# Kernel tuning notes

Hardware: AMD Instinct MI355X
Metric: run time of the kernel (lower is better)

## Reference

```python
import jax, jax.numpy as jnp
import numpy as np

N_NODES = 50000


def _gin_conv(x, src, dst, w1, b1, w2, b2):
    # sum-aggregate neighbor features: agg[i] = sum_{(j->i) in E} x[j]
    agg = jax.ops.segment_sum(x[src], dst, num_segments=N_NODES)
    h = x + agg  # eps = 0 (PyG GINConv default, not trainable)
    h = jnp.maximum(h @ w1 + b1, 0.0) @ w2 + b2
    return h


def setup_inputs() -> dict:
    key = jax.random.key(0)
    ks = jax.random.split(key, 10)
    d_in, d_h, d_out = 128, 256, 2
    E = 600000
    x = jax.random.normal(ks[0], (N_NODES, d_in), dtype=jnp.float32)
    edge_index = jax.random.randint(ks[1], (2, E), 0, N_NODES, dtype=jnp.int64)
    s = lambda k, sh: jax.random.normal(k, sh, dtype=jnp.float32) * (1.0 / np.sqrt(sh[0]))
    return {
        "x": x,
        "edge_index": edge_index,
        "w1": s(ks[2], (d_in, d_h)), "b1": jnp.zeros((d_h,), jnp.float32),
        "w2": s(ks[3], (d_h, d_h)), "b2": jnp.zeros((d_h,), jnp.float32),
        "w3": s(ks[4], (d_h, d_h)), "b3": jnp.zeros((d_h,), jnp.float32),
        "w4": s(ks[5], (d_h, d_out)), "b4": jnp.zeros((d_out,), jnp.float32),
    }


def reference(x, edge_index, w1, b1, w2, b2, w3, b3, w4, b4):
    src, dst = edge_index[0], edge_index[1]
    h = _gin_conv(x, src, dst, w1, b1, w2, b2)
    h = jnp.maximum(h, 0.0)  # F.relu between the two GINConv layers
    h = _gin_conv(h, src, dst, w3, b3, w4, b4)
    return jax.nn.log_softmax(h, axis=1)
```

## Files before the change

### kernel.cpp

```cpp
#include <hip/hip_runtime.h>
#include <hip/hip_bf16.h>


typedef __attribute__((ext_vector_type(8))) short bf16x8;
typedef __attribute__((ext_vector_type(4))) float f32x4;

static __device__ __forceinline__ unsigned short f2bf(float f) {
    unsigned int u = __float_as_uint(f);
    unsigned int r = (u + 0x7fffu + ((u >> 16) & 1u)) >> 16;
    return (unsigned short)r;
}
static __device__ __forceinline__ float bf2f(unsigned short s) {
    return __uint_as_float(((unsigned int)s) << 16);
}
static __device__ __forceinline__ float bflo(unsigned int u) {
    return __uint_as_float(u << 16);
}
static __device__ __forceinline__ float bfhi(unsigned int u) {
    return __uint_as_float(u & 0xffff0000u);
}

#define S1 136
#define S2 264

__global__ __launch_bounds__(256) void degree_kernel(
    const int* __restrict__ dst, int* __restrict__ deg, int E)
{
    const int e = blockIdx.x * 256 + threadIdx.x;
    if (e < E) atomicAdd(&deg[dst[e]], 1);
}

__global__ __launch_bounds__(256) void block_sum_kernel(
    const int* __restrict__ deg, int* __restrict__ bsum, int M)
{
    const int b = blockIdx.x, t = threadIdx.x;
    const int idx = b * 1024 + t * 4;
    int s = 0;
    if (idx + 3 < M) {
        const int4 v = *(const int4*)(deg + idx);
        s = v.x + v.y + v.z + v.w;
    } else {
        #pragma unroll
        for (int i = 0; i < 4; ++i) if (idx + i < M) s += deg[idx + i];
    }
    #pragma unroll
    for (int off = 32; off > 0; off >>= 1) s += __shfl_down(s, off);
    __shared__ int ws[4];
    if ((t & 63) == 0) ws[t >> 6] = s;
    __syncthreads();
    if (t == 0) bsum[b] = ws[0] + ws[1] + ws[2] + ws[3];
}

__global__ __launch_bounds__(64) void scan_partials_kernel(
    const int* __restrict__ bsum, int* __restrict__ boff, int nB)
{
    const int t = threadIdx.x;
    const int v = (t < nB) ? bsum[t] : 0;
    int inc = v;
    #pragma unroll
    for (int off = 1; off < 64; off <<= 1) {
        const int u = __shfl_up(inc, off);
        if (t >= off) inc += u;
    }
    if (t < nB) boff[t] = inc - v;
}

__global__ __launch_bounds__(256) void scan_blocks_kernel(
    const int* __restrict__ deg, const int* __restrict__ boff,
    int* __restrict__ rowptr, int* __restrict__ cur, int M, int E)
{
    const int b = blockIdx.x, t = threadIdx.x;
    const int idx = b * 1024 + t * 4;
    int4 d = make_int4(0, 0, 0, 0);
    if (idx + 3 < M) {
        d = *(const int4*)(deg + idx);
    } else {
        if (idx + 0 < M) d.x = deg[idx + 0];
        if (idx + 1 < M) d.y = deg[idx + 1];
        if (idx + 2 < M) d.z = deg[idx + 2];
        if (idx + 3 < M) d.w = deg[idx + 3];
    }
    const int tot = d.x + d.y + d.z + d.w;
    const int lane = t & 63, wid = t >> 6;
    int inc = tot;
    #pragma unroll
    for (int off = 1; off < 64; off <<= 1) {
        const int u = __shfl_up(inc, off);
        if (lane >= off) inc += u;
    }
    __shared__ int wsum[4];
    if (lane == 63) wsum[wid] = inc;
    __syncthreads();
    int woff = 0;
    #pragma unroll
    for (int w = 0; w < 4; ++w) if (w < wid) woff += wsum[w];
    int p = boff[b] + woff + (inc - tot);
    if (idx + 0 < M) { rowptr[idx + 0] = p; cur[idx + 0] = p; } p += d.x;
    if (idx + 1 < M) { rowptr[idx + 1] = p; cur[idx + 1] = p; } p += d.y;
    if (idx + 2 < M) { rowptr[idx + 2] = p; cur[idx + 2] = p; } p += d.z;
    if (idx + 3 < M) { rowptr[idx + 3] = p; cur[idx + 3] = p; }
    if (b == 0 && t == 0) rowptr[M] = E;
}

__global__ __launch_bounds__(256) void fill_kernel(
    const int* __restrict__ src, const int* __restrict__ dst,
    int* __restrict__ cur, int* __restrict__ srcs, int E)
{
    const int e = blockIdx.x * 256 + threadIdx.x;
    if (e >= E) return;
    const int p = atomicAdd(&cur[dst[e]], 1);
    srcs[p] = src[e];
}

__global__ __launch_bounds__(256) void cvt_bf16_kernel(
    const float* __restrict__ in, short* __restrict__ outb, int n4)
{
    const int i = (blockIdx.x * 256 + threadIdx.x);
    if (i >= n4) return;
    const float4 v = *(const float4*)(in + (size_t)i * 4);
    ushort4 o;
    o.x = f2bf(v.x); o.y = f2bf(v.y); o.z = f2bf(v.z); o.w = f2bf(v.w);
    *(ushort4*)(outb + (size_t)i * 4) = o;
}

__global__ __launch_bounds__(256) void transpose_cvt_kernel(
    const float* __restrict__ in, short* __restrict__ outb,
    int K, int N, int ostride)
{
    __shared__ float tile[32][33];
    const int k0 = blockIdx.x * 32;
    const int n0 = blockIdx.y * 32;
    const int tx = threadIdx.x & 31;
    const int ty = threadIdx.x >> 5;
    #pragma unroll
    for (int i = 0; i < 4; ++i)
        tile[ty + 8 * i][tx] = in[(size_t)(k0 + ty + 8 * i) * N + n0 + tx];
    __syncthreads();
    #pragma unroll
    for (int i = 0; i < 4; ++i)
        outb[(size_t)(n0 + ty + 8 * i) * ostride + k0 + tx] = (short)f2bf(tile[tx][ty + 8 * i]);
}

__global__ __launch_bounds__(256) void gather_add_d128(
    const short* __restrict__ feat,
    const int* __restrict__ rowptr, const int* __restrict__ srcs,
    short* __restrict__ outb, int M)
{
    const int row = blockIdx.x * 4 + (threadIdx.x >> 6);
    if (row >= M) return;
    const int o = (threadIdx.x & 63) * 2;
    const unsigned int u = *(const unsigned int*)(feat + (size_t)row * 128 + o);
    float a0 = bflo(u), a1 = bfhi(u);
    const int jb = rowptr[row], je = rowptr[row + 1];
    int j = jb;
    for (; j + 4 <= je; j += 4) {
        const int s0 = srcs[j + 0];
        const int s1 = srcs[j + 1];
        const int s2 = srcs[j + 2];
        const int s3 = srcs[j + 3];
        const unsigned int v0 = *(const unsigned int*)(feat + (size_t)s0 * 128 + o);
        const unsigned int v1 = *(const unsigned int*)(feat + (size_t)s1 * 128 + o);
        const unsigned int v2 = *(const unsigned int*)(feat + (size_t)s2 * 128 + o);
        const unsigned int v3 = *(const unsigned int*)(feat + (size_t)s3 * 128 + o);
        a0 += bflo(v0); a1 += bfhi(v0);
        a0 += bflo(v1); a1 += bfhi(v1);
        a0 += bflo(v2); a1 += bfhi(v2);
        a0 += bflo(v3); a1 += bfhi(v3);
    }
    for (; j < je; ++j) {
        const int s = srcs[j];
        const unsigned int v = *(const unsigned int*)(feat + (size_t)s * 128 + o);
        a0 += bflo(v); a1 += bfhi(v);
    }
    const unsigned int up = (unsigned int)f2bf(a0) | ((unsigned int)f2bf(a1) << 16);
    *(unsigned int*)(outb + (size_t)row * S1 + o) = up;
}

__global__ __launch_bounds__(256) void gather_add_d256(
    const short* __restrict__ feat,
    const int* __restrict__ rowptr, const int* __restrict__ srcs,
    short* __restrict__ outb, int M)
{
    const int row = blockIdx.x * 4 + (threadIdx.x >> 6);
    if (row >= M) return;
    const int o = (threadIdx.x & 63) * 4;
    const uint2 u = *(const uint2*)(feat + (size_t)row * 256 + o);
    float a0 = bflo(u.x), a1 = bfhi(u.x);
    float a2 = bflo(u.y), a3 = bfhi(u.y);
    const int jb = rowptr[row], je = rowptr[row + 1];
    int j = jb;
    for (; j + 4 <= je; j += 4) {
        const int s0 = srcs[j + 0];
        const int s1 = srcs[j + 1];
        const int s2 = srcs[j + 2];
        const int s3 = srcs[j + 3];
        const uint2 v0 = *(const uint2*)(feat + (size_t)s0 * 256 + o);
        const uint2 v1 = *(const uint2*)(feat + (size_t)s1 * 256 + o);
        const uint2 v2 = *(const uint2*)(feat + (size_t)s2 * 256 + o);
        const uint2 v3 = *(const uint2*)(feat + (size_t)s3 * 256 + o);
        a0 += bflo(v0.x); a1 += bfhi(v0.x); a2 += bflo(v0.y); a3 += bfhi(v0.y);
        a0 += bflo(v1.x); a1 += bfhi(v1.x); a2 += bflo(v1.y); a3 += bfhi(v1.y);
        a0 += bflo(v2.x); a1 += bfhi(v2.x); a2 += bflo(v2.y); a3 += bfhi(v2.y);
        a0 += bflo(v3.x); a1 += bfhi(v3.x); a2 += bflo(v3.y); a3 += bfhi(v3.y);
    }
    for (; j < je; ++j) {
        const int s = srcs[j];
        const uint2 v = *(const uint2*)(feat + (size_t)s * 256 + o);
        a0 += bflo(v.x); a1 += bfhi(v.x); a2 += bflo(v.y); a3 += bfhi(v.y);
    }
    uint2 up;
    up.x = (unsigned int)f2bf(a0) | ((unsigned int)f2bf(a1) << 16);
    up.y = (unsigned int)f2bf(a2) | ((unsigned int)f2bf(a3) << 16);
    *(uint2*)(outb + (size_t)row * S2 + o) = up;
}

__global__ __launch_bounds__(256) void layer1_fused(
    const short* __restrict__ h1in,
    const short* __restrict__ w1t,
    const float* __restrict__ b1,
    const short* __restrict__ w2t,
    const float* __restrict__ b2,
    short* __restrict__ h1,
    int M)
{
    __shared__ short sT[64 * S2];
    const int tid  = threadIdx.x;
    const int lane = tid & 63;
    const int wid  = tid >> 6;
    const int r16  = lane & 15;
    const int q    = lane >> 4;
    const int tm   = blockIdx.x * 64;
    const int wn   = wid * 64;

    f32x4 acc[4][4];
    #pragma unroll
    for (int i = 0; i < 4; ++i)
        #pragma unroll
        for (int j = 0; j < 4; ++j)
            acc[i][j] = (f32x4)0.f;

    const short* Abase = h1in + (size_t)tm * S1;
    #pragma unroll
    for (int k0 = 0; k0 < 128; k0 += 32) {
        bf16x8 af[4], bfr[4];
        #pragma unroll
        for (int i = 0; i < 4; ++i)
            af[i] = *(const bf16x8*)(Abase + (size_t)(i * 16 + r16) * S1 + k0 + q * 8);
        #pragma unroll
        for (int j = 0; j < 4; ++j)
            bfr[j] = *(const bf16x8*)(w1t + (size_t)(wn + j * 16 + r16) * S1 + k0 + q * 8);
        #pragma unroll
        for (int i = 0; i < 4; ++i)
            #pragma unroll
            for (int j = 0; j < 4; ++j)
                acc[i][j] = __builtin_amdgcn_mfma_f32_16x16x32_bf16(af[i], bfr[j], acc[i][j], 0, 0, 0);
    }

    #pragma unroll
    for (int j = 0; j < 4; ++j) {
        const int col = wn + j * 16 + r16;
        const float bj = b1[col];
        #pragma unroll
        for (int i = 0; i < 4; ++i)
            #pragma unroll
            for (int r = 0; r < 4; ++r) {
                float v = fmaxf(acc[i][j][r] + bj, 0.f);
                sT[(i * 16 + q * 4 + r) * S2 + col] = (short)f2bf(v);
            }
    }
    __syncthreads();

    #pragma unroll
    for (int i = 0; i < 4; ++i)
        #pragma unroll
        for (int j = 0; j < 4; ++j)
            acc[i][j] = (f32x4)0.f;

    #pragma unroll
    for (int k0 = 0; k0 < 256; k0 += 32) {
        bf16x8 af[4], bfr[4];
        #pragma unroll
        for (int i = 0; i < 4; ++i)
            af[i] = *(const bf16x8*)(&sT[(i * 16 + r16) * S2 + k0 + q * 8]);
        #pragma unroll
        for (int j = 0; j < 4; ++j)
            bfr[j] = *(const bf16x8*)(w2t + (size_t)(wn + j * 16 + r16) * S2 + k0 + q * 8);
        #pragma unroll
        for (int i = 0; i < 4; ++i)
            #pragma unroll
            for (int j = 0; j < 4; ++j)
                acc[i][j] = __builtin_amdgcn_mfma_f32_16x16x32_bf16(af[i], bfr[j], acc[i][j], 0, 0, 0);
    }
    __syncthreads();

    #pragma unroll
    for (int j = 0; j < 4; ++j) {
        const int col = wn + j * 16 + r16;
        const float bj = b2[col];
        #pragma unroll
        for (int i = 0; i < 4; ++i)
            #pragma unroll
            for (int r = 0; r < 4; ++r) {
                float v = fmaxf(acc[i][j][r] + bj, 0.f);
                sT[(i * 16 + q * 4 + r) * S2 + col] = (short)f2bf(v);
            }
    }
    __syncthreads();

    #pragma unroll
    for (int c = 0; c < 8; ++c) {
        const int idx = tid + c * 256;
        const int row = idx >> 5;
        const int ch  = idx & 31;
        const int rg  = tm + row;
        if (rg < M) {
            const uint4 v = *(const uint4*)(&sT[row * S2 + ch * 8]);
            *(uint4*)(h1 + (size_t)rg * 256 + ch * 8) = v;
        }
    }
}

__global__ __launch_bounds__(256) void layer2_fused(
    const short* __restrict__ h2in,
    const short* __restrict__ w3t,
    const float* __restrict__ b3,
    const float* __restrict__ w4,
    const float* __restrict__ b4,
    float* __restrict__ out,
    int M)
{
    __shared__ short sT[64 * S2];
    const int tid  = threadIdx.x;
    const int lane = tid & 63;
    const int wid  = tid >> 6;
    const int r16  = lane & 15;
    const int q    = lane >> 4;
    const int tm   = blockIdx.x * 64;
    const int wn   = wid * 64;

    f32x4 acc[4][4];
    #pragma unroll
    for (int i = 0; i < 4; ++i)
        #pragma unroll
        for (int j = 0; j < 4; ++j)
            acc[i][j] = (f32x4)0.f;

    const short* Abase = h2in + (size_t)tm * S2;
    #pragma unroll
    for (int k0 = 0; k0 < 256; k0 += 32) {
        bf16x8 af[4], bfr[4];
        #pragma unroll
        for (int i = 0; i < 4; ++i)
            af[i] = *(const bf16x8*)(Abase + (size_t)(i * 16 + r16) * S2 + k0 + q * 8);
        #pragma unroll
        for (int j = 0; j < 4; ++j)
            bfr[j] = *(const bf16x8*)(w3t + (size_t)(wn + j * 16 + r16) * S2 + k0 + q * 8);
        #pragma unroll
        for (int i = 0; i < 4; ++i)
            #pragma unroll
            for (int j = 0; j < 4; ++j)
                acc[i][j] = __builtin_amdgcn_mfma_f32_16x16x32_bf16(af[i], bfr[j], acc[i][j], 0, 0, 0);
    }

    #pragma unroll
    for (int j = 0; j < 4; ++j) {
        const int col = wn + j * 16 + r16;
        const float bj = b3[col];
        #pragma unroll
        for (int i = 0; i < 4; ++i)
            #pragma unroll
            for (int r = 0; r < 4; ++r) {
                float v = fmaxf(acc[i][j][r] + bj, 0.f);
                sT[(i * 16 + q * 4 + r) * S2 + col] = (short)f2bf(v);
            }
    }
    __syncthreads();

    const int row = tid >> 2;
    const int qd  = tid & 3;
    const short* tp = &sT[row * S2 + qd * 64];
    const float* w4p = w4 + qd * 128;
    float s0 = 0.f, s1 = 0.f;
    #pragma unroll 8
    for (int k = 0; k < 64; ++k) {
        const float a = bf2f((unsigned short)tp[k]);
        const float2 w = *(const float2*)(w4p + 2 * k);
        s0 = fmaf(a, w.x, s0);
        s1 = fmaf(a, w.y, s1);
    }
    s0 += __shfl_down(s0, 2, 4);  s1 += __shfl_down(s1, 2, 4);
    s0 += __shfl_down(s0, 1, 4);  s1 += __shfl_down(s1, 1, 4);
    if (qd == 0) {
        const int rg = tm + row;
        if (rg < M) {
            s0 += b4[0];
            s1 += b4[1];
            const float m = fmaxf(s0, s1);
            const float l = logf(__expf(s0 - m) + __expf(s1 - m));
            float2 o;
            o.x = s0 - m - l;
            o.y = s1 - m - l;
            *(float2*)(out + (size_t)rg * 2) = o;
        }
    }
}

extern "C" void kernel_launch(void* const* d_in, const int* in_sizes, int n_in,
                              void* d_out, int out_size, void* d_ws, size_t ws_size,
                              hipStream_t stream)
{
    const float* x  = (const float*)d_in[0];
    const int*   ei = (const int*)d_in[1];
    const float* w1 = (const float*)d_in[2];
    const float* b1 = (const float*)d_in[3];
    const float* w2 = (const float*)d_in[4];
    const float* b2 = (const float*)d_in[5];
    const float* w3 = (const float*)d_in[6];
    const float* b3 = (const float*)d_in[7];
    const float* w4 = (const float*)d_in[8];
    const float* b4 = (const float*)d_in[9];

    const int DIN = 128, DH = 256;
    const int M = in_sizes[0] / DIN;
    const int E = in_sizes[1] / 2;
    const int* src = ei;
    const int* dst = ei + E;
    const int nB = (M + 1023) / 1024;

    int* deg    = (int*)d_ws;
    int* cur    = deg + M;
    int* rowptr = cur + M;
    int* bsum   = rowptr + (M + 1);
    int* boff   = bsum + 64;
    int* srcs   = boff + 64;
    size_t off = ((size_t)(3 * M + 1 + 128 + E) * sizeof(int) + 255) & ~(size_t)255;
    short* x_bf = (short*)((char*)d_ws + off);  off += (size_t)M * DIN * 2;
    off = (off + 255) & ~(size_t)255;
    short* h1in = (short*)((char*)d_ws + off);  off += (size_t)M * S1 * 2;
    off = (off + 255) & ~(size_t)255;
    short* h1   = (short*)((char*)d_ws + off);  off += (size_t)M * DH * 2;
    off = (off + 255) & ~(size_t)255;
    short* h2in = (short*)((char*)d_ws + off);  off += (size_t)M * S2 * 2;
    off = (off + 255) & ~(size_t)255;
    short* w1t  = (short*)((char*)d_ws + off);  off += (size_t)DH * S1 * 2;
    off = (off + 255) & ~(size_t)255;
    short* w2t  = (short*)((char*)d_ws + off);  off += (size_t)DH * S2 * 2;
    off = (off + 255) & ~(size_t)255;
    short* w3t  = (short*)((char*)d_ws + off);  off += (size_t)DH * S2 * 2;

    hipMemsetAsync(deg, 0, (size_t)M * sizeof(int), stream);
    degree_kernel<<<(E + 255) / 256, 256, 0, stream>>>(dst, deg, E);
    block_sum_kernel<<<nB, 256, 0, stream>>>(deg, bsum, M);
    scan_partials_kernel<<<1, 64, 0, stream>>>(bsum, boff, nB);
    scan_blocks_kernel<<<nB, 256, 0, stream>>>(deg, boff, rowptr, cur, M, E);
    fill_kernel<<<(E + 255) / 256, 256, 0, stream>>>(src, dst, cur, srcs, E);

    cvt_bf16_kernel<<<((M * DIN / 4) + 255) / 256, 256, 0, stream>>>(x, x_bf, M * DIN / 4);
    transpose_cvt_kernel<<<dim3(DIN / 32, DH / 32), 256, 0, stream>>>(w1, w1t, DIN, DH, S1);
    transpose_cvt_kernel<<<dim3(DH / 32, DH / 32), 256, 0, stream>>>(w2, w2t, DH, DH, S2);
    transpose_cvt_kernel<<<dim3(DH / 32, DH / 32), 256, 0, stream>>>(w3, w3t, DH, DH, S2);

    const int nblk = (M + 63) / 64;

    gather_add_d128<<<(M + 3) / 4, 256, 0, stream>>>(x_bf, rowptr, srcs, h1in, M);
    layer1_fused<<<nblk, 256, 0, stream>>>(h1in, w1t, b1, w2t, b2, h1, M);

    gather_add_d256<<<(M + 3) / 4, 256, 0, stream>>>(h1, rowptr, srcs, h2in, M);
    layer2_fused<<<nblk, 256, 0, stream>>>(h2in, w3t, b3, w4, b4, (float*)d_out, M);
}
```

Before: 296.4 us.

## Fuse neighbor gather-aggregation into layer MLP kernels via shared memory

Each fused layer kernel now gathers and sums neighbor features for its 64-row tile directly into shared memory, then runs the MFMA GEMMs from that buffer. This removes the separate gather kernels and the global round-trip of the aggregated h1in/h2in intermediates. The three weight transpose launches are merged into one 3D-grid launch, and launch bounds now request 4 blocks per CU. The tradeoff is that the irregular gather now runs inside the GEMM kernel with only 782 blocks, which may reduce the latency hiding the standalone gather kernels had from their larger grids.

```diff
diff --git a/kernel.cpp b/kernel.cpp
--- a/kernel.cpp
+++ b/kernel.cpp
@@ -123,13 +123,20 @@
     *(ushort4*)(outb + (size_t)i * 4) = o;
 }
 
-__global__ __launch_bounds__(256) void transpose_cvt_kernel(
-    const float* __restrict__ in, short* __restrict__ outb,
-    int K, int N, int ostride)
-{
+__global__ __launch_bounds__(256) void transpose_cvt3_kernel(
+    const float* __restrict__ w1, const float* __restrict__ w2, const float* __restrict__ w3,
+    short* __restrict__ w1t, short* __restrict__ w2t, short* __restrict__ w3t)
+{
+    const int z = blockIdx.z;
+    const float* in; short* outb; int K, ostride;
+    if (z == 0)      { in = w1; outb = w1t; K = 128; ostride = S1; }
+    else if (z == 1) { in = w2; outb = w2t; K = 256; ostride = S2; }
+    else             { in = w3; outb = w3t; K = 256; ostride = S2; }
+    const int N = 256;
+    const int k0 = blockIdx.x * 32;
+    if (k0 >= K) return;
+    const int n0 = blockIdx.y * 32;
     __shared__ float tile[32][33];
-    const int k0 = blockIdx.x * 32;
-    const int n0 = blockIdx.y * 32;
     const int tx = threadIdx.x & 31;
     const int ty = threadIdx.x >> 5;
     #pragma unroll
@@ -141,81 +148,9 @@
         outb[(size_t)(n0 + ty + 8 * i) * ostride + k0 + tx] = (short)f2bf(tile[tx][ty + 8 * i]);
 }
 
-__global__ __launch_bounds__(256) void gather_add_d128(
-    const short* __restrict__ feat,
+__global__ __launch_bounds__(256, 4) void layer1_fused(
+    const short* __restrict__ x_bf,
     const int* __restrict__ rowptr, const int* __restrict__ srcs,
-    short* __restrict__ outb, int M)
-{
-    const int row = blockIdx.x * 4 + (threadIdx.x >> 6);
-    if (row >= M) return;
-    const int o = (threadIdx.x & 63) * 2;
-    const unsigned int u = *(const unsigned int*)(feat + (size_t)row * 128 + o);
-    float a0 = bflo(u), a1 = bfhi(u);
-    const int jb = rowptr[row], je = rowptr[row + 1];
-    int j = jb;
-    for (; j + 4 <= je; j += 4) {
-        const int s0 = srcs[j + 0];
-        const int s1 = srcs[j + 1];
-        const int s2 = srcs[j + 2];
-        const int s3 = srcs[j + 3];
-        const unsigned int v0 = *(const unsigned int*)(feat + (size_t)s0 * 128 + o);
-        const unsigned int v1 = *(const unsigned int*)(feat + (size_t)s1 * 128 + o);
-        const unsigned int v2 = *(const unsigned int*)(feat + (size_t)s2 * 128 + o);
-        const unsigned int v3 = *(const unsigned int*)(feat + (size_t)s3 * 128 + o);
-        a0 += bflo(v0); a1 += bfhi(v0);
-        a0 += bflo(v1); a1 += bfhi(v1);
-        a0 += bflo(v2); a1 += bfhi(v2);
-        a0 += bflo(v3); a1 += bfhi(v3);
-    }
-    for (; j < je; ++j) {
-        const int s = srcs[j];
-        const unsigned int v = *(const unsigned int*)(feat + (size_t)s * 128 + o);
-        a0 += bflo(v); a1 += bfhi(v);
-    }
-    const unsigned int up = (unsigned int)f2bf(a0) | ((unsigned int)f2bf(a1) << 16);
-    *(unsigned int*)(outb + (size_t)row * S1 + o) = up;
-}
-
-__global__ __launch_bounds__(256) void gather_add_d256(
-    const short* __restrict__ feat,
-    const int* __restrict__ rowptr, const int* __restrict__ srcs,
-    short* __restrict__ outb, int M)
-{
-    const int row = blockIdx.x * 4 + (threadIdx.x >> 6);
-    if (row >= M) return;
-    const int o = (threadIdx.x & 63) * 4;
-    const uint2 u = *(const uint2*)(feat + (size_t)row * 256 + o);
-    float a0 = bflo(u.x), a1 = bfhi(u.x);
-    float a2 = bflo(u.y), a3 = bfhi(u.y);
-    const int jb = rowptr[row], je = rowptr[row + 1];
-    int j = jb;
-    for (; j + 4 <= je; j += 4) {
-        const int s0 = srcs[j + 0];
-        const int s1 = srcs[j + 1];
-        const int s2 = srcs[j + 2];
-        const int s3 = srcs[j + 3];
-        const uint2 v0 = *(const uint2*)(feat + (size_t)s0 * 256 + o);
-        const uint2 v1 = *(const uint2*)(feat + (size_t)s1 * 256 + o);
-        const uint2 v2 = *(const uint2*)(feat + (size_t)s2 * 256 + o);
-        const uint2 v3 = *(const uint2*)(feat + (size_t)s3 * 256 + o);
-        a0 += bflo(v0.x); a1 += bfhi(v0.x); a2 += bflo(v0.y); a3 += bfhi(v0.y);
-        a0 += bflo(v1.x); a1 += bfhi(v1.x); a2 += bflo(v1.y); a3 += bfhi(v1.y);
-        a0 += bflo(v2.x); a1 += bfhi(v2.x); a2 += bflo(v2.y); a3 += bfhi(v2.y);
-        a0 += bflo(v3.x); a1 += bfhi(v3.x); a2 += bflo(v3.y); a3 += bfhi(v3.y);
-    }
-    for (; j < je; ++j) {
-        const int s = srcs[j];
-        const uint2 v = *(const uint2*)(feat + (size_t)s * 256 + o);
-        a0 += bflo(v.x); a1 += bfhi(v.x); a2 += bflo(v.y); a3 += bfhi(v.y);
-    }
-    uint2 up;
-    up.x = (unsigned int)f2bf(a0) | ((unsigned int)f2bf(a1) << 16);
-    up.y = (unsigned int)f2bf(a2) | ((unsigned int)f2bf(a3) << 16);
-    *(uint2*)(outb + (size_t)row * S2 + o) = up;
-}
-
-__global__ __launch_bounds__(256) void layer1_fused(
-    const short* __restrict__ h1in,
     const short* __restrict__ w1t,
     const float* __restrict__ b1,
     const short* __restrict__ w2t,
@@ -223,7 +158,7 @@
     short* __restrict__ h1,
     int M)
 {
-    __shared__ short sT[64 * S2];
+    __shared__ short sBuf[64 * S2];
     const int tid  = threadIdx.x;
     const int lane = tid & 63;
     const int wid  = tid >> 6;
@@ -232,6 +167,42 @@
     const int tm   = blockIdx.x * 64;
     const int wn   = wid * 64;
 
+    {
+        const int o = lane * 2;
+        for (int rr = 0; rr < 16; ++rr) {
+            const int r = wid * 16 + rr;
+            const int rg = tm + r;
+            float a0 = 0.f, a1 = 0.f;
+            if (rg < M) {
+                const unsigned int u = *(const unsigned int*)(x_bf + (size_t)rg * 128 + o);
+                a0 = bflo(u); a1 = bfhi(u);
+                const int jb = rowptr[rg], je = rowptr[rg + 1];
+                int j = jb;
+                for (; j + 4 <= je; j += 4) {
+                    const int s0 = srcs[j + 0];
+                    const int s1 = srcs[j + 1];
+                    const int s2 = srcs[j + 2];
+                    const int s3 = srcs[j + 3];
+                    const unsigned int v0 = *(const unsigned int*)(x_bf + (size_t)s0 * 128 + o);
+                    const unsigned int v1 = *(const unsigned int*)(x_bf + (size_t)s1 * 128 + o);
+                    const unsigned int v2 = *(const unsigned int*)(x_bf + (size_t)s2 * 128 + o);
+                    const unsigned int v3 = *(const unsigned int*)(x_bf + (size_t)s3 * 128 + o);
+                    a0 += bflo(v0); a1 += bfhi(v0);
+                    a0 += bflo(v1); a1 += bfhi(v1);
+                    a0 += bflo(v2); a1 += bfhi(v2);
+                    a0 += bflo(v3); a1 += bfhi(v3);
+                }
+                for (; j < je; ++j) {
+                    const unsigned int v = *(const unsigned int*)(x_bf + (size_t)srcs[j] * 128 + o);
+                    a0 += bflo(v); a1 += bfhi(v);
+                }
+            }
+            const unsigned int up = (unsigned int)f2bf(a0) | ((unsigned int)f2bf(a1) << 16);
+            *(unsigned int*)(&sBuf[r * S1 + o]) = up;
+        }
+    }
+    __syncthreads();
+
     f32x4 acc[4][4];
     #pragma unroll
     for (int i = 0; i < 4; ++i)
@@ -239,13 +210,12 @@
         for (int j = 0; j < 4; ++j)
             acc[i][j] = (f32x4)0.f;
 
-    const short* Abase = h1in + (size_t)tm * S1;
     #pragma unroll
     for (int k0 = 0; k0 < 128; k0 += 32) {
         bf16x8 af[4], bfr[4];
         #pragma unroll
         for (int i = 0; i < 4; ++i)
-            af[i] = *(const bf16x8*)(Abase + (size_t)(i * 16 + r16) * S1 + k0 + q * 8);
+            af[i] = *(const bf16x8*)(&sBuf[(i * 16 + r16) * S1 + k0 + q * 8]);
         #pragma unroll
         for (int j = 0; j < 4; ++j)
             bfr[j] = *(const bf16x8*)(w1t + (size_t)(wn + j * 16 + r16) * S1 + k0 + q * 8);
@@ -255,6 +225,7 @@
             for (int j = 0; j < 4; ++j)
                 acc[i][j] = __builtin_amdgcn_mfma_f32_16x16x32_bf16(af[i], bfr[j], acc[i][j], 0, 0, 0);
     }
+    __syncthreads();
 
     #pragma unroll
     for (int j = 0; j < 4; ++j) {
@@ -265,7 +236,7 @@
             #pragma unroll
             for (int r = 0; r < 4; ++r) {
                 float v = fmaxf(acc[i][j][r] + bj, 0.f);
-                sT[(i * 16 + q * 4 + r) * S2 + col] = (short)f2bf(v);
+                sBuf[(i * 16 + q * 4 + r) * S2 + col] = (short)f2bf(v);
             }
     }
     __syncthreads();
@@ -281,7 +252,7 @@
         bf16x8 af[4], bfr[4];
         #pragma unroll
         for (int i = 0; i < 4; ++i)
-            af[i] = *(const bf16x8*)(&sT[(i * 16 + r16) * S2 + k0 + q * 8]);
+            af[i] = *(const bf16x8*)(&sBuf[(i * 16 + r16) * S2 + k0 + q * 8]);
         #pragma unroll
         for (int j = 0; j < 4; ++j)
             bfr[j] = *(const bf16x8*)(w2t + (size_t)(wn + j * 16 + r16) * S2 + k0 + q * 8);
@@ -302,7 +273,7 @@
             #pragma unroll
             for (int r = 0; r < 4; ++r) {
                 float v = fmaxf(acc[i][j][r] + bj, 0.f);
-                sT[(i * 16 + q * 4 + r) * S2 + col] = (short)f2bf(v);
+                sBuf[(i * 16 + q * 4 + r) * S2 + col] = (short)f2bf(v);
             }
     }
     __syncthreads();
@@ -314,14 +285,15 @@
         const int ch  = idx & 31;
         const int rg  = tm + row;
         if (rg < M) {
-            const uint4 v = *(const uint4*)(&sT[row * S2 + ch * 8]);
+            const uint4 v = *(const uint4*)(&sBuf[row * S2 + ch * 8]);
             *(uint4*)(h1 + (size_t)rg * 256 + ch * 8) = v;
         }
     }
 }
 
-__global__ __launch_bounds__(256) void layer2_fused(
-    const short* __restrict__ h2in,
+__global__ __launch_bounds__(256, 4) void layer2_fused(
+    const short* __restrict__ h1,
+    const int* __restrict__ rowptr, const int* __restrict__ srcs,
     const short* __restrict__ w3t,
     const float* __restrict__ b3,
     const float* __restrict__ w4,
@@ -329,7 +301,7 @@
     float* __restrict__ out,
     int M)
 {
-    __shared__ short sT[64 * S2];
+    __shared__ short sBuf[64 * S2];
     const int tid  = threadIdx.x;
     const int lane = tid & 63;
     const int wid  = tid >> 6;
@@ -338,6 +310,44 @@
     const int tm   = blockIdx.x * 64;
     const int wn   = wid * 64;
 
+    {
+        const int o = lane * 4;
+        for (int rr = 0; rr < 16; ++rr) {
+            const int r = wid * 16 + rr;
+            const int rg = tm + r;
+            float a0 = 0.f, a1 = 0.f, a2 = 0.f, a3 = 0.f;
+            if (rg < M) {
+                const uint2 u = *(const uint2*)(h1 + (size_t)rg * 256 + o);
+                a0 = bflo(u.x); a1 = bfhi(u.x); a2 = bflo(u.y); a3 = bfhi(u.y);
+                const int jb = rowptr[rg], je = rowptr[rg + 1];
+                int j = jb;
+                for (; j + 4 <= je; j += 4) {
+                    const int s0 = srcs[j + 0];
+                    const int s1 = srcs[j + 1];
+                    const int s2 = srcs[j + 2];
+                    const int s3 = srcs[j + 3];
+                    const uint2 v0 = *(const uint2*)(h1 + (size_t)s0 * 256 + o);
+                    const uint2 v1 = *(const uint2*)(h1 + (size_t)s1 * 256 + o);
+                    const uint2 v2 = *(const uint2*)(h1 + (size_t)s2 * 256 + o);
+                    const uint2 v3 = *(const uint2*)(h1 + (size_t)s3 * 256 + o);
+                    a0 += bflo(v0.x); a1 += bfhi(v0.x); a2 += bflo(v0.y); a3 += bfhi(v0.y);
+                    a0 += bflo(v1.x); a1 += bfhi(v1.x); a2 += bflo(v1.y); a3 += bfhi(v1.y);
+                    a0 += bflo(v2.x); a1 += bfhi(v2.x); a2 += bflo(v2.y); a3 += bfhi(v2.y);
+                    a0 += bflo(v3.x); a1 += bfhi(v3.x); a2 += bflo(v3.y); a3 += bfhi(v3.y);
+                }
+                for (; j < je; ++j) {
+                    const uint2 v = *(const uint2*)(h1 + (size_t)srcs[j] * 256 + o);
+                    a0 += bflo(v.x); a1 += bfhi(v.x); a2 += bflo(v.y); a3 += bfhi(v.y);
+                }
+            }
+            uint2 up;
+            up.x = (unsigned int)f2bf(a0) | ((unsigned int)f2bf(a1) << 16);
+            up.y = (unsigned int)f2bf(a2) | ((unsigned int)f2bf(a3) << 16);
+            *(uint2*)(&sBuf[r * S2 + o]) = up;
+        }
+    }
+    __syncthreads();
+
     f32x4 acc[4][4];
     #pragma unroll
     for (int i = 0; i < 4; ++i)
@@ -345,13 +355,12 @@
         for (int j = 0; j < 4; ++j)
             acc[i][j] = (f32x4)0.f;
 
-    const short* Abase = h2in + (size_t)tm * S2;
     #pragma unroll
     for (int k0 = 0; k0 < 256; k0 += 32) {
         bf16x8 af[4], bfr[4];
         #pragma unroll
         for (int i = 0; i < 4; ++i)
-            af[i] = *(const bf16x8*)(Abase + (size_t)(i * 16 + r16) * S2 + k0 + q * 8);
+            af[i] = *(const bf16x8*)(&sBuf[(i * 16 + r16) * S2 + k0 + q * 8]);
         #pragma unroll
         for (int j = 0; j < 4; ++j)
             bfr[j] = *(const bf16x8*)(w3t + (size_t)(wn + j * 16 + r16) * S2 + k0 + q * 8);
@@ -361,6 +370,7 @@
             for (int j = 0; j < 4; ++j)
                 acc[i][j] = __builtin_amdgcn_mfma_f32_16x16x32_bf16(af[i], bfr[j], acc[i][j], 0, 0, 0);
     }
+    __syncthreads();
 
     #pragma unroll
     for (int j = 0; j < 4; ++j) {
@@ -371,14 +381,14 @@
             #pragma unroll
             for (int r = 0; r < 4; ++r) {
                 float v = fmaxf(acc[i][j][r] + bj, 0.f);
-                sT[(i * 16 + q * 4 + r) * S2 + col] = (short)f2bf(v);
+                sBuf[(i * 16 + q * 4 + r) * S2 + col] = (short)f2bf(v);
             }
     }
     __syncthreads();
 
     const int row = tid >> 2;
     const int qd  = tid & 3;
-    const short* tp = &sT[row * S2 + qd * 64];
+    const short* tp = &sBuf[row * S2 + qd * 64];
     const float* w4p = w4 + qd * 128;
     float s0 = 0.f, s1 = 0.f;
     #pragma unroll 8
@@ -436,11 +446,7 @@
     size_t off = ((size_t)(3 * M + 1 + 128 + E) * sizeof(int) + 255) & ~(size_t)255;
     short* x_bf = (short*)((char*)d_ws + off);  off += (size_t)M * DIN * 2;
     off = (off + 255) & ~(size_t)255;
-    short* h1in = (short*)((char*)d_ws + off);  off += (size_t)M * S1 * 2;
-    off = (off + 255) & ~(size_t)255;
     short* h1   = (short*)((char*)d_ws + off);  off += (size_t)M * DH * 2;
-    off = (off + 255) & ~(size_t)255;
-    short* h2in = (short*)((char*)d_ws + off);  off += (size_t)M * S2 * 2;
     off = (off + 255) & ~(size_t)255;
     short* w1t  = (short*)((char*)d_ws + off);  off += (size_t)DH * S1 * 2;
     off = (off + 255) & ~(size_t)255;
@@ -456,15 +462,10 @@
     fill_kernel<<<(E + 255) / 256, 256, 0, stream>>>(src, dst, cur, srcs, E);
 
     cvt_bf16_kernel<<<((M * DIN / 4) + 255) / 256, 256, 0, stream>>>(x, x_bf, M * DIN / 4);
-    transpose_cvt_kernel<<<dim3(DIN / 32, DH / 32), 256, 0, stream>>>(w1, w1t, DIN, DH, S1);
-    transpose_cvt_kernel<<<dim3(DH / 32, DH / 32), 256, 0, stream>>>(w2, w2t, DH, DH, S2);
-    transpose_cvt_kernel<<<dim3(DH / 32, DH / 32), 256, 0, stream>>>(w3, w3t, DH, DH, S2);
+    transpose_cvt3_kernel<<<dim3(8, 8, 3), 256, 0, stream>>>(w1, w2, w3, w1t, w2t, w3t);
 
     const int nblk = (M + 63) / 64;
 
-    gather_add_d128<<<(M + 3) / 4, 256, 0, stream>>>(x_bf, rowptr, srcs, h1in, M);
-    layer1_fused<<<nblk, 256, 0, stream>>>(h1in, w1t, b1, w2t, b2, h1, M);
-
-    gather_add_d256<<<(M + 3) / 4, 256, 0, stream>>>(h1, rowptr, srcs, h2in, M);
-    layer2_fused<<<nblk, 256, 0, stream>>>(h2in, w3t, b3, w4, b4, (float*)d_out, M);
-}
+    layer1_fused<<<nblk, 256, 0, stream>>>(x_bf, rowptr, srcs, w1t, b1, w2t, b2, h1, M);
+    layer2_fused<<<nblk, 256, 0, stream>>>(h1, rowptr, srcs, w3t, b3, w4, b4, (float*)d_out, M);
+}
```

New measurement: 318.0 us. 1.07x slower.
